# Kernel tuning notes

Hardware: AMD Instinct MI355X
Metric: run time of the kernel (lower is better)

Reference implementation:

```python
import jax, jax.numpy as jnp
import numpy as np

BATCH = 15
SEQ = 4096
N_IN = 512
N_H = 1024


def setup_inputs() -> dict:
    key = jax.random.key(0)
    ks = jax.random.split(key, 7)
    s_ih = 1.0 / np.sqrt(N_H)
    return {
        "x": jax.random.normal(ks[0], (BATCH, SEQ, N_IN), dtype=jnp.float32),
        "W_ih": jax.random.uniform(ks[1], (N_H, N_IN), jnp.float32, -s_ih, s_ih),
        "b_ih": jax.random.uniform(ks[2], (N_H,), jnp.float32, -s_ih, s_ih),
        "W_hh": jax.random.uniform(ks[3], (N_H, N_H), jnp.float32, -s_ih, s_ih),
        "b_hh": jax.random.uniform(ks[4], (N_H,), jnp.float32, -s_ih, s_ih),
        "W_fc": jax.random.uniform(ks[5], (1, N_H), jnp.float32, -s_ih, s_ih),
        "b_fc": jax.random.uniform(ks[6], (1,), jnp.float32, -s_ih, s_ih),
    }


def reference(x, W_ih, b_ih, W_hh, b_hh, W_fc, b_fc):
    # x: [B, T, F] -> time-major [T, B, F]
    xt = jnp.swapaxes(x, 0, 1)
    # Precompute input projections for all timesteps in one big GEMM.
    x_proj = jnp.einsum("tbf,hf->tbh", xt, W_ih) + b_ih + b_hh  # [T, B, H]
    h0 = jnp.zeros((BATCH, N_H), dtype=x.dtype)

    def step(h, xp):
        h_new = jnp.tanh(xp + h @ W_hh.T)
        return h_new, None

    h_final, _ = jax.lax.scan(step, h0, x_proj)
    out = jax.nn.sigmoid(h_final @ W_fc.T + b_fc)  # [B, 1]
    return out
```

## Files before the change

### kernel.cpp

```cpp
#include <hip/hip_runtime.h>
#include <hip/hip_bf16.h>
#include <stdint.h>

typedef unsigned int u32;
typedef unsigned long long u64;
typedef __attribute__((ext_vector_type(8))) short short8;
typedef __attribute__((ext_vector_type(4))) float floatx4;

#define T_STEPS 4096
#define BATCH   15
#define N_IN    512
#define N_H     1024
#define G_LAUNCH 64
#define THREADS 512
#define LDS_ROW 516

#define OFF_XP    0
#define OFF_WIHB  (134217728)
#define OFF_HBUF  (134217728 + 1048576)
#define OFF_FLAGS (134217728 + 1048576 + 65536)
#define OFF_CLAIM (134217728 + 1048576 + 65536 + 4096)

__device__ inline u32 f2bf1(float f) {
    u32 u = __builtin_bit_cast(u32, f);
    return (u + 0x7FFFu + ((u >> 16) & 1u)) >> 16;
}
__device__ inline float bf2f(u32 us) {
    return __builtin_bit_cast(float, us << 16);
}
__device__ inline float tanh_fast(float x) {
    float e = __expf(2.0f * x);
    return 1.0f - 2.0f / (e + 1.0f);
}
__device__ inline u64 mb_load(const u64* p) {
    return __hip_atomic_load(p, __ATOMIC_RELAXED, __HIP_MEMORY_SCOPE_AGENT);
}
__device__ inline void pub_store32(u32* p, u32 v) {
    __hip_atomic_store(p, v, __ATOMIC_RELAXED, __HIP_MEMORY_SCOPE_WORKGROUP);
}
__device__ inline void pub_store64(u64* p, u64 v) {
    __hip_atomic_store(p, v, __ATOMIC_RELAXED, __HIP_MEMORY_SCOPE_WORKGROUP);
}
__device__ inline void release_fence() {
    asm volatile("s_waitcnt vmcnt(0)" ::: "memory");
}

__global__ void k_cvt_wih(const float* __restrict__ W_ih, u32* __restrict__ wihb,
                          u32* __restrict__ claim, u32* __restrict__ hbuf,
                          u64* __restrict__ fl) {
    int row = blockIdx.x;
    int tid = threadIdx.x;
    if (row == 0 && tid < 16) claim[tid] = 0;
    if (row == 0 && tid >= 16 && tid < 80)
        __hip_atomic_exchange(fl + (size_t)(tid - 16) * 8, 0ull,
                              __ATOMIC_RELAXED, __HIP_MEMORY_SCOPE_AGENT);
    if ((row == 1 || row == 2) && tid < 256) {
        u64* hz = (u64*)(hbuf + ((size_t)(row - 1) * 16 + 15) * 512);
        __hip_atomic_exchange(hz + tid, 0ull,
                              __ATOMIC_RELAXED, __HIP_MEMORY_SCOPE_AGENT);
    }
    const float* p = W_ih + (size_t)row * N_IN + tid * 2;
    u32 packed = f2bf1(p[0]) | (f2bf1(p[1]) << 16);
    wihb[row * (N_IN / 2) + tid] = packed;
}

__global__ void __launch_bounds__(256) k_xproj(
        const float* __restrict__ x, const u32* __restrict__ wihb,
        const float* __restrict__ b_ih, const float* __restrict__ b_hh,
        u64* __restrict__ xp) {
    const int t     = blockIdx.x;
    const int slice = blockIdx.y;
    const int tid   = threadIdx.x;
    const int wave  = tid >> 6;
    const int l     = tid & 63;
    const int row   = l & 15;
    const int quad  = l >> 4;
    const int colbase = slice * 256 + wave * 64;

    floatx4 acc[4] = {{0,0,0,0},{0,0,0,0},{0,0,0,0},{0,0,0,0}};
    const float* xrow = x + ((size_t)row * T_STEPS + t) * N_IN;

    #pragma unroll
    for (int kk = 0; kk < 16; ++kk) {
        short8 a;
        if (row < 15) {
            const float* pa = xrow + kk * 32 + quad * 8;
            float4 x0 = *(const float4*)(pa);
            float4 x1 = *(const float4*)(pa + 4);
            a[0]=(short)f2bf1(x0.x); a[1]=(short)f2bf1(x0.y); a[2]=(short)f2bf1(x0.z); a[3]=(short)f2bf1(x0.w);
            a[4]=(short)f2bf1(x1.x); a[5]=(short)f2bf1(x1.y); a[6]=(short)f2bf1(x1.z); a[7]=(short)f2bf1(x1.w);
        } else {
            #pragma unroll
            for (int j = 0; j < 8; ++j) a[j] = 0;
        }
        #pragma unroll
        for (int c4 = 0; c4 < 4; ++c4) {
            int col = colbase + c4 * 16 + (l & 15);
            const uint4* pb = (const uint4*)(wihb + (size_t)col * (N_IN/2) + kk * 16 + quad * 4);
            short8 b = __builtin_bit_cast(short8, *pb);
            acc[c4] = __builtin_amdgcn_mfma_f32_16x16x32_bf16(a, b, acc[c4], 0, 0, 0);
        }
    }
    #pragma unroll
    for (int c4 = 0; c4 < 4; ++c4) {
        int col = colbase + c4 * 16 + (l & 15);
        float bias = b_ih[col] + b_hh[col];
        u64 packed = (u64)f2bf1(acc[c4][0] + bias)
                   | ((u64)f2bf1(acc[c4][1] + bias) << 16)
                   | ((u64)f2bf1(acc[c4][2] + bias) << 32)
                   | ((u64)f2bf1(acc[c4][3] + bias) << 48);
        int cw = slice * 16 + wave * 4 + c4;
        xp[((size_t)t * 64 + cw) * 64 + l] = packed;
    }
}

__global__ void __launch_bounds__(THREADS, 2) k_scan(
        const float* __restrict__ W_hh, const u64* __restrict__ xp,
        u32* __restrict__ hbuf, u64* __restrict__ fl, u32* __restrict__ claim,
        const float* __restrict__ W_fc, const float* __restrict__ b_fc,
        float* __restrict__ out) {
    __shared__ u32 h_lds[2][16 * LDS_ROW];
    __shared__ float red[256];
    __shared__ int s_slot;
    __shared__ int s_dead;

    const int tid  = threadIdx.x;
    const int wave = tid >> 6;
    const int l    = tid & 63;
    const int c    = l & 15;
    const int quad = l >> 4;

    if (tid == 0) {
        u32 xcd;
        asm volatile("s_getreg_b32 %0, hwreg(HW_REG_XCC_ID)" : "=s"(xcd));
        xcd &= 7u;
        u32 slot = __hip_atomic_fetch_add(&claim[xcd], 1u, __ATOMIC_RELAXED,
                                          __HIP_MEMORY_SCOPE_AGENT);
        if (slot == 7u) {
            u32 exp = 0u;
            __hip_atomic_compare_exchange_strong(&claim[8], &exp, xcd + 1u,
                __ATOMIC_RELAXED, __ATOMIC_RELAXED, __HIP_MEMORY_SCOPE_AGENT);
        }
        u32 w = 0; int gg = 0;
        do { w = __hip_atomic_load(&claim[8], __ATOMIC_RELAXED, __HIP_MEMORY_SCOPE_AGENT); }
        while (!w && ++gg < (1 << 22));
        s_slot = (w == xcd + 1u && slot < 8u) ? (int)slot : -1;
        s_dead = 0;
    }
    __syncthreads();
    const int g = s_slot;
    if (g < 0) return;

    const int col  = g * 128 + wave * 16 + c;
    const int cw   = g * 8 + wave;
    const int wgf  = g * 8 + wave;

    short8 wf[32];
    {
        const float* wr = W_hh + (size_t)col * N_H;
        #pragma unroll
        for (int kk = 0; kk < 32; ++kk) {
            const float* p = wr + kk * 32 + quad * 8;
            float4 w0 = *(const float4*)(p);
            float4 w1 = *(const float4*)(p + 4);
            short8 bfr;
            bfr[0]=(short)f2bf1(w0.x); bfr[1]=(short)f2bf1(w0.y); bfr[2]=(short)f2bf1(w0.z); bfr[3]=(short)f2bf1(w0.w);
            bfr[4]=(short)f2bf1(w1.x); bfr[5]=(short)f2bf1(w1.y); bfr[6]=(short)f2bf1(w1.z); bfr[7]=(short)f2bf1(w1.w);
            wf[kk] = bfr;
        }
    }
    for (int i = tid; i < 2 * 16 * LDS_ROW; i += THREADS) ((u32*)h_lds)[i] = 0;
    __syncthreads();

    u64 xpw = xp[((size_t)0 * 64 + cw) * 64 + l];
    u64 xpw_n = xp[((size_t)1 * 64 + cw) * 64 + l];
    float h[4];
    {
        h[0] = tanh_fast(bf2f((u32)(xpw      ) & 0xFFFFu));
        h[1] = tanh_fast(bf2f((u32)(xpw >> 16) & 0xFFFFu));
        h[2] = tanh_fast(bf2f((u32)(xpw >> 32) & 0xFFFFu));
        h[3] = tanh_fast(bf2f((u32)(xpw >> 48) & 0xFFFFu));
        u32* bufw = hbuf + (size_t)1 * (16 * 512);
        #pragma unroll
        for (int i = 0; i < 4; ++i) {
            int bt = quad * 4 + i;
            float o = __shfl_xor(h[i], 1);
            if (!(c & 1) && bt < 15) {
                u32 data = f2bf1(h[i]) | (f2bf1(o) << 16);
                pub_store32(bufw + bt * 512 + (col >> 1), data);
            }
        }
        release_fence();
        if (l == 0) pub_store64(fl + (size_t)wgf * 8, 1ull);
    }

    for (int s = 1; s < T_STEPS; ++s) {
        xpw = xpw_n;
        const int par = s & 1;
        u32* lds = &h_lds[par][0];

        {
            const u64 want = (u64)s;
            int rounds = 0;
            while (true) {
                u64 f = mb_load(fl + (size_t)l * 8);
                if (__all((int)(f >= want))) break;
                if (++rounds > (1 << 20)) { s_dead = 1; break; }
            }
        }

        {
            const u64* src = (const u64*)(hbuf + (size_t)par * (16 * 512));
            u64 d0 = mb_load(src + tid +    0), d1 = mb_load(src + tid +  512);
            u64 d2 = mb_load(src + tid + 1024), d3 = mb_load(src + tid + 1536);
            u64 d4 = mb_load(src + tid + 2048), d5 = mb_load(src + tid + 2560);
            u64 d6 = mb_load(src + tid + 3072), d7 = mb_load(src + tid + 3584);
            const int rbase = tid >> 8;
            const int cc    = (tid & 255) * 2;
            *(u64*)(lds + (size_t)(rbase +  0) * LDS_ROW + cc) = d0;
            *(u64*)(lds + (size_t)(rbase +  2) * LDS_ROW + cc) = d1;
            *(u64*)(lds + (size_t)(rbase +  4) * LDS_ROW + cc) = d2;
            *(u64*)(lds + (size_t)(rbase +  6) * LDS_ROW + cc) = d3;
            *(u64*)(lds + (size_t)(rbase +  8) * LDS_ROW + cc) = d4;
            *(u64*)(lds + (size_t)(rbase + 10) * LDS_ROW + cc) = d5;
            *(u64*)(lds + (size_t)(rbase + 12) * LDS_ROW + cc) = d6;
            *(u64*)(lds + (size_t)(rbase + 14) * LDS_ROW + cc) = d7;
        }
        __syncthreads();
        if (s_dead) break;

        if (s + 1 < T_STEPS) xpw_n = xp[((size_t)(s + 1) * 64 + cw) * 64 + l];

        floatx4 acc0, acc1;
        acc0[0] = bf2f((u32)(xpw      ) & 0xFFFFu);
        acc0[1] = bf2f((u32)(xpw >> 16) & 0xFFFFu);
        acc0[2] = bf2f((u32)(xpw >> 32) & 0xFFFFu);
        acc0[3] = bf2f((u32)(xpw >> 48) & 0xFFFFu);
        acc1[0] = 0.f; acc1[1] = 0.f; acc1[2] = 0.f; acc1[3] = 0.f;

        #pragma unroll
        for (int t = 0; t < 16; ++t) {
            uint4 a0 = *(const uint4*)&lds[c * LDS_ROW + (2 * t    ) * 16 + quad * 4];
            uint4 a1 = *(const uint4*)&lds[c * LDS_ROW + (2 * t + 1) * 16 + quad * 4];
            acc0 = __builtin_amdgcn_mfma_f32_16x16x32_bf16(
                       __builtin_bit_cast(short8, a0), wf[2 * t    ], acc0, 0, 0, 0);
            acc1 = __builtin_amdgcn_mfma_f32_16x16x32_bf16(
                       __builtin_bit_cast(short8, a1), wf[2 * t + 1], acc1, 0, 0, 0);
        }

        #pragma unroll
        for (int i = 0; i < 4; ++i) h[i] = tanh_fast(acc0[i] + acc1[i]);

        asm volatile("" :: "v"(xpw_n));

        u32* bufw = hbuf + (size_t)((s + 1) & 1) * (16 * 512);
        #pragma unroll
        for (int i = 0; i < 4; ++i) {
            int bt = quad * 4 + i;
            float o = __shfl_xor(h[i], 1);
            if (!(c & 1) && bt < 15) {
                u32 data = f2bf1(h[i]) | (f2bf1(o) << 16);
                pub_store32(bufw + bt * 512 + (col >> 1), data);
            }
        }
        release_fence();
        if (l == 0) pub_store64(fl + (size_t)wgf * 8, (u64)(s + 1));
    }

    if (g == 0) {
        if (!s_dead) {
            const u64 want = (u64)T_STEPS;
            int rounds = 0;
            while (true) {
                u64 f = mb_load(fl + (size_t)l * 8);
                if (__all((int)(f >= want))) break;
                if (++rounds > (1 << 20)) break;
            }
            u32* lds = &h_lds[0][0];
            const u64* src = (const u64*)(hbuf + (size_t)0);
            u64 d0 = mb_load(src + tid +    0), d1 = mb_load(src + tid +  512);
            u64 d2 = mb_load(src + tid + 1024), d3 = mb_load(src + tid + 1536);
            u64 d4 = mb_load(src + tid + 2048), d5 = mb_load(src + tid + 2560);
            u64 d6 = mb_load(src + tid + 3072), d7 = mb_load(src + tid + 3584);
            const int rbase = tid >> 8;
            const int cc    = (tid & 255) * 2;
            *(u64*)(lds + (size_t)(rbase +  0) * LDS_ROW + cc) = d0;
            *(u64*)(lds + (size_t)(rbase +  2) * LDS_ROW + cc) = d1;
            *(u64*)(lds + (size_t)(rbase +  4) * LDS_ROW + cc) = d2;
            *(u64*)(lds + (size_t)(rbase +  6) * LDS_ROW + cc) = d3;
            *(u64*)(lds + (size_t)(rbase +  8) * LDS_ROW + cc) = d4;
            *(u64*)(lds + (size_t)(rbase + 10) * LDS_ROW + cc) = d5;
            *(u64*)(lds + (size_t)(rbase + 12) * LDS_ROW + cc) = d6;
            *(u64*)(lds + (size_t)(rbase + 14) * LDS_ROW + cc) = d7;
        }
        __syncthreads();
        u32* lds = &h_lds[0][0];
        if (tid < 240) {
            int b = tid >> 4, seg = tid & 15;
            float sum = 0.f;
            for (int j = 0; j < 64; ++j) {
                int k = seg * 64 + j;
                u32 pr = lds[b * LDS_ROW + (k >> 1)];
                float hv = bf2f((pr >> ((k & 1) * 16)) & 0xFFFFu);
                sum += hv * W_fc[k];
            }
            red[tid] = sum;
        }
        __syncthreads();
        if (tid < 15) {
            float z = 0.f;
            #pragma unroll
            for (int j = 0; j < 16; ++j) z += red[tid * 16 + j];
            z += b_fc[0];
            out[tid] = 1.0f / (1.0f + __expf(-z));
        }
    }
}

extern "C" void kernel_launch(void* const* d_in, const int* in_sizes, int n_in,
                              void* d_out, int out_size, void* d_ws, size_t ws_size,
                              hipStream_t stream) {
    const float* x    = (const float*)d_in[0];
    const float* W_ih = (const float*)d_in[1];
    const float* b_ih = (const float*)d_in[2];
    const float* W_hh = (const float*)d_in[3];
    const float* b_hh = (const float*)d_in[4];
    const float* W_fc = (const float*)d_in[5];
    const float* b_fc = (const float*)d_in[6];
    float* out = (float*)d_out;

    char* ws    = (char*)d_ws;
    u64*  xp    = (u64*)(ws + OFF_XP);
    u32*  wihb  = (u32*)(ws + OFF_WIHB);
    u32*  hbuf  = (u32*)(ws + OFF_HBUF);
    u64*  fl    = (u64*)(ws + OFF_FLAGS);
    u32*  claim = (u32*)(ws + OFF_CLAIM);

    k_cvt_wih<<<dim3(N_H), dim3(256), 0, stream>>>(W_ih, wihb, claim, hbuf, fl);
    k_xproj<<<dim3(T_STEPS, 4), dim3(256), 0, stream>>>(x, wihb, b_ih, b_hh, xp);
    k_scan<<<dim3(G_LAUNCH), dim3(THREADS), 0, stream>>>(W_hh, xp, hbuf, fl, claim, W_fc, b_fc, out);
}
```

Before: 11.67 ms.

## Halve scan workgroup to 4 waves, each computing two 16-column tiles

The recurrent scan kernel now runs 256 threads per workgroup instead of 512. Each wave holds two W_hh fragment sets in registers and issues four MFMA chains per k-step, reusing each LDS A-fragment for two column tiles. This halves the number of per-step flags to poll (32 instead of 64) and the number of waves that must sync per step. The cost is doubled register pressure per wave (64 short8 weight fragments), fewer waves to hide latency, and twice the per-thread loads when copying h into LDS.

Result: slower. 13.01 ms (+11.4%).

```diff
diff --git a/kernel.cpp b/kernel.cpp
--- a/kernel.cpp
+++ b/kernel.cpp
@@ -12,7 +12,7 @@
 #define N_IN    512
 #define N_H     1024
 #define G_LAUNCH 64
-#define THREADS 512
+#define THREADS 256
 #define LDS_ROW 516
 
 #define OFF_XP    0
@@ -51,7 +51,7 @@
     int row = blockIdx.x;
     int tid = threadIdx.x;
     if (row == 0 && tid < 16) claim[tid] = 0;
-    if (row == 0 && tid >= 16 && tid < 80)
+    if (row == 0 && tid >= 16 && tid < 48)
         __hip_atomic_exchange(fl + (size_t)(tid - 16) * 8, 0ull,
                               __ATOMIC_RELAXED, __HIP_MEMORY_SCOPE_AGENT);
     if ((row == 1 || row == 2) && tid < 256) {
@@ -114,7 +114,7 @@
     }
 }
 
-__global__ void __launch_bounds__(THREADS, 2) k_scan(
+__global__ void __launch_bounds__(THREADS, 1) k_scan(
         const float* __restrict__ W_hh, const u64* __restrict__ xp,
         u32* __restrict__ hbuf, u64* __restrict__ fl, u32* __restrict__ claim,
         const float* __restrict__ W_fc, const float* __restrict__ b_fc,
@@ -125,7 +125,7 @@
     __shared__ int s_dead;
 
     const int tid  = threadIdx.x;
-    const int wave = tid >> 6;
+    const int w    = tid >> 6;
     const int l    = tid & 63;
     const int c    = l & 15;
     const int quad = l >> 4;
@@ -141,53 +141,62 @@
             __hip_atomic_compare_exchange_strong(&claim[8], &exp, xcd + 1u,
                 __ATOMIC_RELAXED, __ATOMIC_RELAXED, __HIP_MEMORY_SCOPE_AGENT);
         }
-        u32 w = 0; int gg = 0;
-        do { w = __hip_atomic_load(&claim[8], __ATOMIC_RELAXED, __HIP_MEMORY_SCOPE_AGENT); }
-        while (!w && ++gg < (1 << 22));
-        s_slot = (w == xcd + 1u && slot < 8u) ? (int)slot : -1;
+        u32 ww = 0; int gg = 0;
+        do { ww = __hip_atomic_load(&claim[8], __ATOMIC_RELAXED, __HIP_MEMORY_SCOPE_AGENT); }
+        while (!ww && ++gg < (1 << 22));
+        s_slot = (ww == xcd + 1u && slot < 8u) ? (int)slot : -1;
         s_dead = 0;
     }
     __syncthreads();
     const int g = s_slot;
     if (g < 0) return;
 
-    const int col  = g * 128 + wave * 16 + c;
-    const int cw   = g * 8 + wave;
-    const int wgf  = g * 8 + wave;
-
-    short8 wf[32];
+    const int colbase = g * 128 + w * 32;
+    const int cw0  = g * 8 + w * 2;
+    const int cw1  = cw0 + 1;
+    const int wgf  = g * 4 + w;
+
+    short8 wf0[32], wf1[32];
     {
-        const float* wr = W_hh + (size_t)col * N_H;
         #pragma unroll
         for (int kk = 0; kk < 32; ++kk) {
-            const float* p = wr + kk * 32 + quad * 8;
-            float4 w0 = *(const float4*)(p);
-            float4 w1 = *(const float4*)(p + 4);
-            short8 bfr;
-            bfr[0]=(short)f2bf1(w0.x); bfr[1]=(short)f2bf1(w0.y); bfr[2]=(short)f2bf1(w0.z); bfr[3]=(short)f2bf1(w0.w);
-            bfr[4]=(short)f2bf1(w1.x); bfr[5]=(short)f2bf1(w1.y); bfr[6]=(short)f2bf1(w1.z); bfr[7]=(short)f2bf1(w1.w);
-            wf[kk] = bfr;
+            #pragma unroll
+            for (int t = 0; t < 2; ++t) {
+                int col = colbase + t * 16 + c;
+                const float* p = W_hh + (size_t)col * N_H + kk * 32 + quad * 8;
+                float4 w0 = *(const float4*)(p);
+                float4 w1 = *(const float4*)(p + 4);
+                short8 bfr;
+                bfr[0]=(short)f2bf1(w0.x); bfr[1]=(short)f2bf1(w0.y); bfr[2]=(short)f2bf1(w0.z); bfr[3]=(short)f2bf1(w0.w);
+                bfr[4]=(short)f2bf1(w1.x); bfr[5]=(short)f2bf1(w1.y); bfr[6]=(short)f2bf1(w1.z); bfr[7]=(short)f2bf1(w1.w);
+                if (t == 0) wf0[kk] = bfr; else wf1[kk] = bfr;
+            }
         }
     }
     for (int i = tid; i < 2 * 16 * LDS_ROW; i += THREADS) ((u32*)h_lds)[i] = 0;
     __syncthreads();
 
-    u64 xpw = xp[((size_t)0 * 64 + cw) * 64 + l];
-    u64 xpw_n = xp[((size_t)1 * 64 + cw) * 64 + l];
-    float h[4];
+    u64 xpw0 = xp[((size_t)0 * 64 + cw0) * 64 + l];
+    u64 xpw1 = xp[((size_t)0 * 64 + cw1) * 64 + l];
+    u64 xpn0 = xp[((size_t)1 * 64 + cw0) * 64 + l];
+    u64 xpn1 = xp[((size_t)1 * 64 + cw1) * 64 + l];
+    float h0[4], h1[4];
     {
-        h[0] = tanh_fast(bf2f((u32)(xpw      ) & 0xFFFFu));
-        h[1] = tanh_fast(bf2f((u32)(xpw >> 16) & 0xFFFFu));
-        h[2] = tanh_fast(bf2f((u32)(xpw >> 32) & 0xFFFFu));
-        h[3] = tanh_fast(bf2f((u32)(xpw >> 48) & 0xFFFFu));
+        #pragma unroll
+        for (int i = 0; i < 4; ++i) {
+            h0[i] = tanh_fast(bf2f((u32)(xpw0 >> (16 * i)) & 0xFFFFu));
+            h1[i] = tanh_fast(bf2f((u32)(xpw1 >> (16 * i)) & 0xFFFFu));
+        }
         u32* bufw = hbuf + (size_t)1 * (16 * 512);
         #pragma unroll
         for (int i = 0; i < 4; ++i) {
             int bt = quad * 4 + i;
-            float o = __shfl_xor(h[i], 1);
+            float o0 = __shfl_xor(h0[i], 1);
+            float o1 = __shfl_xor(h1[i], 1);
             if (!(c & 1) && bt < 15) {
-                u32 data = f2bf1(h[i]) | (f2bf1(o) << 16);
-                pub_store32(bufw + bt * 512 + (col >> 1), data);
+                int cb = (colbase + c) >> 1;
+                pub_store32(bufw + bt * 512 + cb,     f2bf1(h0[i]) | (f2bf1(o0) << 16));
+                pub_store32(bufw + bt * 512 + cb + 8, f2bf1(h1[i]) | (f2bf1(o1) << 16));
             }
         }
         release_fence();
@@ -195,7 +204,7 @@
     }
 
     for (int s = 1; s < T_STEPS; ++s) {
-        xpw = xpw_n;
+        xpw0 = xpn0; xpw1 = xpn1;
         const int par = s & 1;
         u32* lds = &h_lds[par][0];
 
@@ -203,7 +212,7 @@
             const u64 want = (u64)s;
             int rounds = 0;
             while (true) {
-                u64 f = mb_load(fl + (size_t)l * 8);
+                u64 f = mb_load(fl + (size_t)(l & 31) * 8);
                 if (__all((int)(f >= want))) break;
                 if (++rounds > (1 << 20)) { s_dead = 1; break; }
             }
@@ -211,56 +220,55 @@
 
         {
             const u64* src = (const u64*)(hbuf + (size_t)par * (16 * 512));
-            u64 d0 = mb_load(src + tid +    0), d1 = mb_load(src + tid +  512);
-            u64 d2 = mb_load(src + tid + 1024), d3 = mb_load(src + tid + 1536);
-            u64 d4 = mb_load(src + tid + 2048), d5 = mb_load(src + tid + 2560);
-            u64 d6 = mb_load(src + tid + 3072), d7 = mb_load(src + tid + 3584);
-            const int rbase = tid >> 8;
-            const int cc    = (tid & 255) * 2;
-            *(u64*)(lds + (size_t)(rbase +  0) * LDS_ROW + cc) = d0;
-            *(u64*)(lds + (size_t)(rbase +  2) * LDS_ROW + cc) = d1;
-            *(u64*)(lds + (size_t)(rbase +  4) * LDS_ROW + cc) = d2;
-            *(u64*)(lds + (size_t)(rbase +  6) * LDS_ROW + cc) = d3;
-            *(u64*)(lds + (size_t)(rbase +  8) * LDS_ROW + cc) = d4;
-            *(u64*)(lds + (size_t)(rbase + 10) * LDS_ROW + cc) = d5;
-            *(u64*)(lds + (size_t)(rbase + 12) * LDS_ROW + cc) = d6;
-            *(u64*)(lds + (size_t)(rbase + 14) * LDS_ROW + cc) = d7;
+            u64 d[16];
+            #pragma unroll
+            for (int k = 0; k < 16; ++k) d[k] = mb_load(src + tid + k * 256);
+            #pragma unroll
+            for (int k = 0; k < 16; ++k)
+                *(u64*)(lds + (size_t)k * LDS_ROW + tid * 2) = d[k];
         }
         __syncthreads();
         if (s_dead) break;
 
-        if (s + 1 < T_STEPS) xpw_n = xp[((size_t)(s + 1) * 64 + cw) * 64 + l];
-
-        floatx4 acc0, acc1;
-        acc0[0] = bf2f((u32)(xpw      ) & 0xFFFFu);
-        acc0[1] = bf2f((u32)(xpw >> 16) & 0xFFFFu);
-        acc0[2] = bf2f((u32)(xpw >> 32) & 0xFFFFu);
-        acc0[3] = bf2f((u32)(xpw >> 48) & 0xFFFFu);
-        acc1[0] = 0.f; acc1[1] = 0.f; acc1[2] = 0.f; acc1[3] = 0.f;
-
+        if (s + 1 < T_STEPS) {
+            xpn0 = xp[((size_t)(s + 1) * 64 + cw0) * 64 + l];
+            xpn1 = xp[((size_t)(s + 1) * 64 + cw1) * 64 + l];
+        }
+
+        floatx4 a00 = {0,0,0,0}, a01 = {0,0,0,0};
+        floatx4 a10 = {0,0,0,0}, a11 = {0,0,0,0};
         #pragma unroll
         for (int t = 0; t < 16; ++t) {
-            uint4 a0 = *(const uint4*)&lds[c * LDS_ROW + (2 * t    ) * 16 + quad * 4];
-            uint4 a1 = *(const uint4*)&lds[c * LDS_ROW + (2 * t + 1) * 16 + quad * 4];
-            acc0 = __builtin_amdgcn_mfma_f32_16x16x32_bf16(
-                       __builtin_bit_cast(short8, a0), wf[2 * t    ], acc0, 0, 0, 0);
-            acc1 = __builtin_amdgcn_mfma_f32_16x16x32_bf16(
-                       __builtin_bit_cast(short8, a1), wf[2 * t + 1], acc1, 0, 0, 0);
-        }
-
-        #pragma unroll
-        for (int i = 0; i < 4; ++i) h[i] = tanh_fast(acc0[i] + acc1[i]);
-
-        asm volatile("" :: "v"(xpw_n));
+            uint4 A0 = *(const uint4*)&lds[c * LDS_ROW + (2 * t    ) * 16 + quad * 4];
+            uint4 A1 = *(const uint4*)&lds[c * LDS_ROW + (2 * t + 1) * 16 + quad * 4];
+            a00 = __builtin_amdgcn_mfma_f32_16x16x32_bf16(
+                      __builtin_bit_cast(short8, A0), wf0[2 * t    ], a00, 0, 0, 0);
+            a10 = __builtin_amdgcn_mfma_f32_16x16x32_bf16(
+                      __builtin_bit_cast(short8, A0), wf1[2 * t    ], a10, 0, 0, 0);
+            a01 = __builtin_amdgcn_mfma_f32_16x16x32_bf16(
+                      __builtin_bit_cast(short8, A1), wf0[2 * t + 1], a01, 0, 0, 0);
+            a11 = __builtin_amdgcn_mfma_f32_16x16x32_bf16(
+                      __builtin_bit_cast(short8, A1), wf1[2 * t + 1], a11, 0, 0, 0);
+        }
+
+        #pragma unroll
+        for (int i = 0; i < 4; ++i) {
+            h0[i] = tanh_fast(bf2f((u32)(xpw0 >> (16 * i)) & 0xFFFFu) + a00[i] + a01[i]);
+            h1[i] = tanh_fast(bf2f((u32)(xpw1 >> (16 * i)) & 0xFFFFu) + a10[i] + a11[i]);
+        }
+
+        asm volatile("" :: "v"(xpn0), "v"(xpn1));
 
         u32* bufw = hbuf + (size_t)((s + 1) & 1) * (16 * 512);
         #pragma unroll
         for (int i = 0; i < 4; ++i) {
             int bt = quad * 4 + i;
-            float o = __shfl_xor(h[i], 1);
+            float o0 = __shfl_xor(h0[i], 1);
+            float o1 = __shfl_xor(h1[i], 1);
             if (!(c & 1) && bt < 15) {
-                u32 data = f2bf1(h[i]) | (f2bf1(o) << 16);
-                pub_store32(bufw + bt * 512 + (col >> 1), data);
+                int cb = (colbase + c) >> 1;
+                pub_store32(bufw + bt * 512 + cb,     f2bf1(h0[i]) | (f2bf1(o0) << 16));
+                pub_store32(bufw + bt * 512 + cb + 8, f2bf1(h1[i]) | (f2bf1(o1) << 16));
             }
         }
         release_fence();
@@ -272,26 +280,18 @@
             const u64 want = (u64)T_STEPS;
             int rounds = 0;
             while (true) {
-                u64 f = mb_load(fl + (size_t)l * 8);
+                u64 f = mb_load(fl + (size_t)(l & 31) * 8);
                 if (__all((int)(f >= want))) break;
                 if (++rounds > (1 << 20)) break;
             }
             u32* lds = &h_lds[0][0];
             const u64* src = (const u64*)(hbuf + (size_t)0);
-            u64 d0 = mb_load(src + tid +    0), d1 = mb_load(src + tid +  512);
-            u64 d2 = mb_load(src + tid + 1024), d3 = mb_load(src + tid + 1536);
-            u64 d4 = mb_load(src + tid + 2048), d5 = mb_load(src + tid + 2560);
-            u64 d6 = mb_load(src + tid + 3072), d7 = mb_load(src + tid + 3584);
-            const int rbase = tid >> 8;
-            const int cc    = (tid & 255) * 2;
-            *(u64*)(lds + (size_t)(rbase +  0) * LDS_ROW + cc) = d0;
-            *(u64*)(lds + (size_t)(rbase +  2) * LDS_ROW + cc) = d1;
-            *(u64*)(lds + (size_t)(rbase +  4) * LDS_ROW + cc) = d2;
-            *(u64*)(lds + (size_t)(rbase +  6) * LDS_ROW + cc) = d3;
-            *(u64*)(lds + (size_t)(rbase +  8) * LDS_ROW + cc) = d4;
-            *(u64*)(lds + (size_t)(rbase + 10) * LDS_ROW + cc) = d5;
-            *(u64*)(lds + (size_t)(rbase + 12) * LDS_ROW + cc) = d6;
-            *(u64*)(lds + (size_t)(rbase + 14) * LDS_ROW + cc) = d7;
+            u64 d[16];
+            #pragma unroll
+            for (int k = 0; k < 16; ++k) d[k] = mb_load(src + tid + k * 256);
+            #pragma unroll
+            for (int k = 0; k < 16; ++k)
+                *(u64*)(lds + (size_t)k * LDS_ROW + tid * 2) = d[k];
         }
         __syncthreads();
         u32* lds = &h_lds[0][0];
```

## Replace per-step block barrier with per-wave LDS flags and sliced h staging

Applied to the files above, without the earlier changes.

Each wave now polls only the 8 producer flags matching its K-slice and copies only the 128-column slice of the hidden state it owns into LDS, skipping the padded 16th batch row. It then publishes a per-wave LDS flag instead of joining a workgroup __syncthreads. Consumers wait on each slice's flag just before the MFMAs that need it, so compute on early slices can start while later slices are still arriving. This removes the full-block barrier from the serial recurrence critical path, at the cost of LDS-flag spinning and more complex memory-ordering assumptions.

Result: slower. 12.63 ms (+8.2%).

```diff
diff --git a/kernel.cpp b/kernel.cpp
--- a/kernel.cpp
+++ b/kernel.cpp
@@ -43,6 +43,9 @@
 }
 __device__ inline void release_fence() {
     asm volatile("s_waitcnt vmcnt(0)" ::: "memory");
+}
+__device__ inline void lds_fence() {
+    asm volatile("s_waitcnt lgkmcnt(0)" ::: "memory");
 }
 
 __global__ void k_cvt_wih(const float* __restrict__ W_ih, u32* __restrict__ wihb,
@@ -120,9 +123,10 @@
         const float* __restrict__ W_fc, const float* __restrict__ b_fc,
         float* __restrict__ out) {
     __shared__ u32 h_lds[2][16 * LDS_ROW];
+    __shared__ u32 sflag[2][8];
     __shared__ float red[256];
     __shared__ int s_slot;
-    __shared__ int s_dead;
+    __shared__ volatile int s_dead_v;
 
     const int tid  = threadIdx.x;
     const int wave = tid >> 6;
@@ -145,8 +149,9 @@
         do { w = __hip_atomic_load(&claim[8], __ATOMIC_RELAXED, __HIP_MEMORY_SCOPE_AGENT); }
         while (!w && ++gg < (1 << 22));
         s_slot = (w == xcd + 1u && slot < 8u) ? (int)slot : -1;
-        s_dead = 0;
-    }
+        s_dead_v = 0;
+    }
+    if (tid < 16) ((u32*)sflag)[tid] = 0;
     __syncthreads();
     const int g = s_slot;
     if (g < 0) return;
@@ -198,36 +203,37 @@
         xpw = xpw_n;
         const int par = s & 1;
         u32* lds = &h_lds[par][0];
+        u32* sf  = &sflag[par][0];
 
         {
             const u64 want = (u64)s;
-            int rounds = 0;
-            while (true) {
-                u64 f = mb_load(fl + (size_t)l * 8);
+            int r = 0;
+            while (!s_dead_v) {
+                u64 f = mb_load(fl + (size_t)(wave * 8 + (l & 7)) * 8);
                 if (__all((int)(f >= want))) break;
-                if (++rounds > (1 << 20)) { s_dead = 1; break; }
-            }
-        }
-
+                if (++r > (1 << 18)) { s_dead_v = 1; break; }
+            }
+        }
         {
-            const u64* src = (const u64*)(hbuf + (size_t)par * (16 * 512));
-            u64 d0 = mb_load(src + tid +    0), d1 = mb_load(src + tid +  512);
-            u64 d2 = mb_load(src + tid + 1024), d3 = mb_load(src + tid + 1536);
-            u64 d4 = mb_load(src + tid + 2048), d5 = mb_load(src + tid + 2560);
-            u64 d6 = mb_load(src + tid + 3072), d7 = mb_load(src + tid + 3584);
-            const int rbase = tid >> 8;
-            const int cc    = (tid & 255) * 2;
-            *(u64*)(lds + (size_t)(rbase +  0) * LDS_ROW + cc) = d0;
-            *(u64*)(lds + (size_t)(rbase +  2) * LDS_ROW + cc) = d1;
-            *(u64*)(lds + (size_t)(rbase +  4) * LDS_ROW + cc) = d2;
-            *(u64*)(lds + (size_t)(rbase +  6) * LDS_ROW + cc) = d3;
-            *(u64*)(lds + (size_t)(rbase +  8) * LDS_ROW + cc) = d4;
-            *(u64*)(lds + (size_t)(rbase + 10) * LDS_ROW + cc) = d5;
-            *(u64*)(lds + (size_t)(rbase + 12) * LDS_ROW + cc) = d6;
-            *(u64*)(lds + (size_t)(rbase + 14) * LDS_ROW + cc) = d7;
-        }
-        __syncthreads();
-        if (s_dead) break;
+            const u64* srcp = (const u64*)(hbuf + (size_t)par * (16 * 512));
+            u64 d[8];
+            #pragma unroll
+            for (int j = 0; j < 8; ++j) {
+                int idx = l + j * 64;
+                if (idx < 480)
+                    d[j] = mb_load(srcp + (size_t)(idx >> 5) * 256 + wave * 32 + (idx & 31));
+            }
+            #pragma unroll
+            for (int j = 0; j < 8; ++j) {
+                int idx = l + j * 64;
+                if (idx < 480)
+                    *(u64*)(lds + (size_t)(idx >> 5) * LDS_ROW + wave * 64 + (idx & 31) * 2) = d[j];
+            }
+            lds_fence();
+            if (l == 0)
+                __hip_atomic_store(&sf[wave], (u32)s, __ATOMIC_RELAXED,
+                                   __HIP_MEMORY_SCOPE_WORKGROUP);
+        }
 
         if (s + 1 < T_STEPS) xpw_n = xp[((size_t)(s + 1) * 64 + cw) * 64 + l];
 
@@ -238,14 +244,32 @@
         acc0[3] = bf2f((u32)(xpw >> 48) & 0xFFFFu);
         acc1[0] = 0.f; acc1[1] = 0.f; acc1[2] = 0.f; acc1[3] = 0.f;
 
-        #pragma unroll
-        for (int t = 0; t < 16; ++t) {
-            uint4 a0 = *(const uint4*)&lds[c * LDS_ROW + (2 * t    ) * 16 + quad * 4];
-            uint4 a1 = *(const uint4*)&lds[c * LDS_ROW + (2 * t + 1) * 16 + quad * 4];
-            acc0 = __builtin_amdgcn_mfma_f32_16x16x32_bf16(
-                       __builtin_bit_cast(short8, a0), wf[2 * t    ], acc0, 0, 0, 0);
-            acc1 = __builtin_amdgcn_mfma_f32_16x16x32_bf16(
-                       __builtin_bit_cast(short8, a1), wf[2 * t + 1], acc1, 0, 0, 0);
+        u32 fn = __hip_atomic_load(&sf[0], __ATOMIC_RELAXED, __HIP_MEMORY_SCOPE_WORKGROUP);
+        #pragma unroll
+        for (int sl = 0; sl < 8; ++sl) {
+            if (fn < (u32)s) {
+                int r = 0;
+                while (!s_dead_v) {
+                    fn = __hip_atomic_load(&sf[sl], __ATOMIC_RELAXED,
+                                           __HIP_MEMORY_SCOPE_WORKGROUP);
+                    if (fn >= (u32)s) break;
+                    if (++r > (1 << 20)) { s_dead_v = 1; break; }
+                }
+            }
+            asm volatile("" ::: "memory");
+            __builtin_amdgcn_sched_barrier(0);
+            if (sl < 7)
+                fn = __hip_atomic_load(&sf[sl + 1], __ATOMIC_RELAXED,
+                                       __HIP_MEMORY_SCOPE_WORKGROUP);
+            #pragma unroll
+            for (int t = 2 * sl; t <= 2 * sl + 1; ++t) {
+                uint4 a0 = *(const uint4*)&lds[c * LDS_ROW + (2 * t    ) * 16 + quad * 4];
+                uint4 a1 = *(const uint4*)&lds[c * LDS_ROW + (2 * t + 1) * 16 + quad * 4];
+                acc0 = __builtin_amdgcn_mfma_f32_16x16x32_bf16(
+                           __builtin_bit_cast(short8, a0), wf[2 * t    ], acc0, 0, 0, 0);
+                acc1 = __builtin_amdgcn_mfma_f32_16x16x32_bf16(
+                           __builtin_bit_cast(short8, a1), wf[2 * t + 1], acc1, 0, 0, 0);
+            }
         }
 
         #pragma unroll
@@ -265,33 +289,34 @@
         }
         release_fence();
         if (l == 0) pub_store64(fl + (size_t)wgf * 8, (u64)(s + 1));
+
+        if (s_dead_v) break;
     }
 
     if (g == 0) {
-        if (!s_dead) {
+        if (!s_dead_v) {
             const u64 want = (u64)T_STEPS;
-            int rounds = 0;
+            int r = 0;
             while (true) {
-                u64 f = mb_load(fl + (size_t)l * 8);
+                u64 f = mb_load(fl + (size_t)(wave * 8 + (l & 7)) * 8);
                 if (__all((int)(f >= want))) break;
-                if (++rounds > (1 << 20)) break;
+                if (++r > (1 << 18)) break;
             }
             u32* lds = &h_lds[0][0];
-            const u64* src = (const u64*)(hbuf + (size_t)0);
-            u64 d0 = mb_load(src + tid +    0), d1 = mb_load(src + tid +  512);
-            u64 d2 = mb_load(src + tid + 1024), d3 = mb_load(src + tid + 1536);
-            u64 d4 = mb_load(src + tid + 2048), d5 = mb_load(src + tid + 2560);
-            u64 d6 = mb_load(src + tid + 3072), d7 = mb_load(src + tid + 3584);
-            const int rbase = tid >> 8;
-            const int cc    = (tid & 255) * 2;
-            *(u64*)(lds + (size_t)(rbase +  0) * LDS_ROW + cc) = d0;
-            *(u64*)(lds + (size_t)(rbase +  2) * LDS_ROW + cc) = d1;
-            *(u64*)(lds + (size_t)(rbase +  4) * LDS_ROW + cc) = d2;
-            *(u64*)(lds + (size_t)(rbase +  6) * LDS_ROW + cc) = d3;
-            *(u64*)(lds + (size_t)(rbase +  8) * LDS_ROW + cc) = d4;
-            *(u64*)(lds + (size_t)(rbase + 10) * LDS_ROW + cc) = d5;
-            *(u64*)(lds + (size_t)(rbase + 12) * LDS_ROW + cc) = d6;
-            *(u64*)(lds + (size_t)(rbase + 14) * LDS_ROW + cc) = d7;
+            const u64* srcp = (const u64*)(hbuf);
+            u64 d[8];
+            #pragma unroll
+            for (int j = 0; j < 8; ++j) {
+                int idx = l + j * 64;
+                if (idx < 480)
+                    d[j] = mb_load(srcp + (size_t)(idx >> 5) * 256 + wave * 32 + (idx & 31));
+            }
+            #pragma unroll
+            for (int j = 0; j < 8; ++j) {
+                int idx = l + j * 64;
+                if (idx < 480)
+                    *(u64*)(lds + (size_t)(idx >> 5) * LDS_ROW + wave * 64 + (idx & 31) * 2) = d[j];
+            }
         }
         __syncthreads();
         u32* lds = &h_lds[0][0];
```
